# Optimization experiments

Hardware: AMD Instinct MI355X
Metric: run time of the kernel (lower is better)

The kernel has to match this reference:

```python
import jax, jax.numpy as jnp
import numpy as np

N_NODES = 100000
N_EDGES = 1600000
K = 3  # TAGConv default hops


def _make_lin(key, out_dim, in_dim):
    # K+1 bias-free linears (stacked) + one shared output bias, per PyG TAGConv
    kw, = jax.random.split(key, 1)
    scale = 1.0 / np.sqrt(in_dim)
    W = jax.random.uniform(kw, (K + 1, out_dim, in_dim), jnp.float32, -scale, scale)
    b = jnp.zeros((out_dim,), jnp.float32)
    return W, b


def setup_inputs() -> dict:
    key = jax.random.key(0)
    ks = jax.random.split(key, 6)
    x = jax.random.normal(ks[0], (N_NODES, 128), jnp.float32)
    edge_index = jax.random.randint(ks[1], (2, N_EDGES), 0, N_NODES, jnp.int64)
    W1, b1 = _make_lin(ks[2], 128, 128)
    W2, b2 = _make_lin(ks[3], 64, 128)
    W3, b3 = _make_lin(ks[4], 16, 64)
    return {"x": x, "edge_index": edge_index, "W1": W1, "b1": b1,
            "W2": W2, "b2": b2, "W3": W3, "b3": b3}


def _tagconv(x, row, col, norm, W, b, n):
    # out = sum_k lin_k(A_norm^k x) + b ; message x_j*norm gathered at col
    out = jnp.einsum('nd,od->no', x, W[0])
    h = x
    for k in range(1, W.shape[0]):
        h = jax.ops.segment_sum(norm[:, None] * h[row], col, num_segments=n)
        out = out + jnp.einsum('nd,od->no', h, W[k])
    return out + b


def _dropout(x, key, p=0.5):
    keep = jax.random.bernoulli(key, 1.0 - p, x.shape)
    return jnp.where(keep, x / (1.0 - p), 0.0)


def reference(x, edge_index, W1, b1, W2, b2, W3, b3):
    n = x.shape[0]
    row, col = edge_index[0], edge_index[1]
    # gcn_norm without self-loops (TAGConv default)
    deg = jax.ops.segment_sum(jnp.ones(row.shape[0], x.dtype), col, num_segments=n)
    dis = jnp.where(deg > 0, 1.0 / jnp.sqrt(jnp.where(deg > 0, deg, 1.0)), 0.0)
    norm = dis[row] * dis[col]

    dk1, dk2 = jax.random.split(jax.random.key(42))
    h = _tagconv(x, row, col, norm, W1, b1, n)
    h = _dropout(h, dk1)
    h = _tagconv(h, row, col, norm, W2, b2, n)
    h = jax.nn.elu(h)
    h = _dropout(h, dk2)
    h = _tagconv(h, row, col, norm, W3, b3, n)
    return h
```

## Files before the change

### kernel.cpp

```cpp
#include <hip/hip_runtime.h>
#include <stdint.h>
#include <math.h>

#define N_NODES 100000
#define N_EDGES 1600000

typedef __bf16 bf16_t;
typedef __attribute__((ext_vector_type(4))) __bf16 bf16x4;
typedef __attribute__((ext_vector_type(8))) __bf16 bf16x8;
typedef __attribute__((ext_vector_type(4))) float f32x4;

__device__ __forceinline__ f32x4 mfma16(bf16x8 a, bf16x8 b, f32x4 c) {
  return __builtin_amdgcn_mfma_f32_16x16x32_bf16(a, b, c, 0, 0, 0);
}

__device__ __host__ __forceinline__ uint32_t rotl32(uint32_t v, int d) {
  return (v << d) | (v >> (32 - d));
}

__device__ __host__ __forceinline__ void threefry2x32(uint32_t k0, uint32_t k1,
                                                      uint32_t x0, uint32_t x1,
                                                      uint32_t& o0, uint32_t& o1) {
  uint32_t ks0 = k0, ks1 = k1, ks2 = k0 ^ k1 ^ 0x1BD11BDAu;
  x0 += ks0; x1 += ks1;
#define TF_R(r) { x0 += x1; x1 = rotl32(x1, r); x1 ^= x0; }
  TF_R(13) TF_R(15) TF_R(26) TF_R(6)
  x0 += ks1; x1 += ks2 + 1u;
  TF_R(17) TF_R(29) TF_R(16) TF_R(24)
  x0 += ks2; x1 += ks0 + 2u;
  TF_R(13) TF_R(15) TF_R(26) TF_R(6)
  x0 += ks0; x1 += ks1 + 3u;
  TF_R(17) TF_R(29) TF_R(16) TF_R(24)
  x0 += ks1; x1 += ks2 + 4u;
  TF_R(13) TF_R(15) TF_R(26) TF_R(6)
  x0 += ks2; x1 += ks0 + 5u;
#undef TF_R
  o0 = x0; o1 = x1;
}

__device__ __forceinline__ float drop_scale(uint32_t idx, uint32_t k0, uint32_t k1) {
  uint32_t o0, o1;
  threefry2x32(k0, k1, 0u, idx, o0, o1);
  uint32_t bits = o0 ^ o1;
  float u = __uint_as_float((bits >> 9) | 0x3f800000u) - 1.0f;
  return (u < 0.5f) ? 2.0f : 0.0f;
}

__global__ __launch_bounds__(256) void detect_kernel(const int* __restrict__ ei,
                                                     int* __restrict__ found_nonzero) {
  int idx = blockIdx.x * 256 + threadIdx.x;
  size_t j = (size_t)idx * 781;
  if (ei[2 * j + 1] != 0) atomicOr(found_nonzero, 1);
}

__device__ __forceinline__ int edge_row(const int* ei, bool i32, int e) {
  return i32 ? ei[e] : ei[2 * (size_t)e];
}
__device__ __forceinline__ int edge_col(const int* ei, bool i32, int e) {
  return i32 ? ei[N_EDGES + e] : ei[2 * ((size_t)N_EDGES + (size_t)e)];
}

__global__ __launch_bounds__(256) void deg_kernel(const int* __restrict__ ei,
                                                  const int* __restrict__ flag,
                                                  int* __restrict__ deg) {
  int e = blockIdx.x * 256 + threadIdx.x;
  if (e < N_EDGES) {
    bool i32 = *flag != 0;
    atomicAdd(&deg[edge_col(ei, i32, e)], 1);
  }
}

__global__ __launch_bounds__(256) void dis_kernel(const int* __restrict__ deg,
                                                  float* __restrict__ dis) {
  int n = blockIdx.x * 256 + threadIdx.x;
  if (n < N_NODES) {
    int d = deg[n];
    dis[n] = (d > 0) ? (1.0f / sqrtf((float)d)) : 0.0f;
  }
}

#define SCAN_NB 391
__global__ __launch_bounds__(256) void bsum_kernel(const int* __restrict__ deg,
                                                   int* __restrict__ bsum) {
  __shared__ int sh[256];
  int i = blockIdx.x * 256 + threadIdx.x;
  sh[threadIdx.x] = (i < N_NODES) ? deg[i] : 0;
  __syncthreads();
  for (int ofs = 128; ofs > 0; ofs >>= 1) {
    if (threadIdx.x < ofs) sh[threadIdx.x] += sh[threadIdx.x + ofs];
    __syncthreads();
  }
  if (threadIdx.x == 0) bsum[blockIdx.x] = sh[0];
}

__global__ __launch_bounds__(512) void bscan_kernel(const int* __restrict__ bsum,
                                                    int* __restrict__ boffs) {
  __shared__ int sh[512];
  int t = threadIdx.x;
  int v = (t < SCAN_NB) ? bsum[t] : 0;
  sh[t] = v;
  __syncthreads();
  for (int ofs = 1; ofs < 512; ofs <<= 1) {
    int u = (t >= ofs) ? sh[t - ofs] : 0;
    __syncthreads();
    sh[t] += u;
    __syncthreads();
  }
  if (t < SCAN_NB) boffs[t] = sh[t] - v;
  if (t == 0) boffs[SCAN_NB] = sh[SCAN_NB - 1];
}

__global__ __launch_bounds__(256) void rptr_kernel(const int* __restrict__ deg,
                                                   const int* __restrict__ boffs,
                                                   int* __restrict__ rptr) {
  __shared__ int sh[256];
  int i = blockIdx.x * 256 + threadIdx.x;
  int v = (i < N_NODES) ? deg[i] : 0;
  sh[threadIdx.x] = v;
  __syncthreads();
  for (int ofs = 1; ofs < 256; ofs <<= 1) {
    int u = (threadIdx.x >= ofs) ? sh[threadIdx.x - ofs] : 0;
    __syncthreads();
    sh[threadIdx.x] += u;
    __syncthreads();
  }
  if (i <= N_NODES) rptr[i] = boffs[blockIdx.x] + sh[threadIdx.x] - v;
}

#define NFILL 512
#define MB1 1563
#define RANGE_N 12500

__device__ void fill_range(int b, int tid, const int* __restrict__ ei,
                           const int* __restrict__ flag,
                           const float* __restrict__ dis,
                           const int* __restrict__ rptr,
                           int* cursor, int2* __restrict__ erec) {
  int g = b & 7;
  int gb = b >> 3;
  int lo = g * RANGE_N, hi = lo + RANGE_N;
  bool i32 = *flag != 0;
  for (int e = gb * 256 + tid; e < N_EDGES; e += 64 * 256) {
    int c = edge_col(ei, i32, e);
    if (c < lo || c >= hi) continue;
    int r = edge_row(ei, i32, e);
    int p = atomicAdd(&cursor[c], 1);
    erec[rptr[c] + p] = make_int2(r, __float_as_int(dis[r] * dis[c]));
  }
}

__global__ __launch_bounds__(256) void fused1_kernel(
    const int* __restrict__ ei, const int* __restrict__ flag,
    const float* __restrict__ dis, const int* __restrict__ rptr,
    int* cursor, int2* __restrict__ erec,
    const float* __restrict__ x, const float* __restrict__ W1f,
    const float* __restrict__ b1,
    float* __restrict__ y0, bf16_t* __restrict__ y1,
    bf16_t* __restrict__ y2, bf16_t* __restrict__ y3,
    const float* __restrict__ W2, const float* __restrict__ W3,
    bf16_t* __restrict__ Wb2, bf16_t* __restrict__ Wb3) {
  constexpr int DIN = 128, LDK = DIN + 8, KI = DIN / 32, NCH = 8;
  __shared__ bf16_t sm[2][64 * LDK];
  const int tid = threadIdx.x;
  int b = blockIdx.x;

  if (b < NFILL) {
    fill_range(b, tid, ei, flag, dis, rptr, cursor, erec);
    return;
  }
  b -= NFILL;
  if (b >= MB1) {
    for (int i = tid; i < 32768; i += 256) Wb2[i] = (bf16_t)W2[i];
    for (int i = tid; i < 4096; i += 256) Wb3[i] = (bf16_t)W3[i];
    return;
  }

  const int m0 = b * 64;
  union U4 { bf16_t b[4]; uint2 u; };
  union U8 { bf16_t b[8]; uint4 u; };
  {
    constexpr int NL = 64 * DIN / 4 / 256;
#pragma unroll
    for (int it = 0; it < NL; ++it) {
      int idx = tid + it * 256;
      int r = idx / (DIN / 4), cc = (idx % (DIN / 4)) * 4;
      int gm = m0 + r;
      float4 v = (gm < N_NODES) ? ((const float4*)x)[((size_t)gm * DIN + cc) >> 2]
                                : make_float4(0.f, 0.f, 0.f, 0.f);
      U4 hi, lo;
      hi.b[0] = (bf16_t)v.x; lo.b[0] = (bf16_t)(v.x - (float)hi.b[0]);
      hi.b[1] = (bf16_t)v.y; lo.b[1] = (bf16_t)(v.y - (float)hi.b[1]);
      hi.b[2] = (bf16_t)v.z; lo.b[2] = (bf16_t)(v.z - (float)hi.b[2]);
      hi.b[3] = (bf16_t)v.w; lo.b[3] = (bf16_t)(v.w - (float)hi.b[3]);
      *(uint2*)&sm[0][r * LDK + cc] = hi.u;
      *(uint2*)&sm[1][r * LDK + cc] = lo.u;
    }
  }
  __syncthreads();

  const int w = tid >> 6, lane = tid & 63;
  const int wm = w & 1, wn = w >> 1;
  const int quad = lane >> 4, lr = lane & 15;

  bf16x8 aH[2][KI], aL[2][KI];
#pragma unroll
  for (int mt = 0; mt < 2; ++mt)
#pragma unroll
    for (int ki = 0; ki < KI; ++ki) {
      int rowa = wm * 32 + mt * 16 + lr;
      int koff = ki * 32 + quad * 8;
      aH[mt][ki] = *(const bf16x8*)&sm[0][rowa * LDK + koff];
      aL[mt][ki] = *(const bf16x8*)&sm[1][rowa * LDK + koff];
    }
  __syncthreads();

  constexpr int NLB = 64 * DIN / 8 / 256;
  auto loadW = [&](int gr, int cc) -> uint4 {
    const float4* p = (const float4*)&W1f[(size_t)gr * DIN + cc];
    float4 a = p[0], bq = p[1];
    U8 t;
    t.b[0] = (bf16_t)a.x;  t.b[1] = (bf16_t)a.y;
    t.b[2] = (bf16_t)a.z;  t.b[3] = (bf16_t)a.w;
    t.b[4] = (bf16_t)bq.x; t.b[5] = (bf16_t)bq.y;
    t.b[6] = (bf16_t)bq.z; t.b[7] = (bf16_t)bq.w;
    return t.u;
  };
  uint4 wreg[NLB];
#pragma unroll
  for (int it = 0; it < NLB; ++it) {
    int idx = tid + it * 256;
    int r = idx / (DIN / 8), cc = (idx % (DIN / 8)) * 8;
    wreg[it] = loadW(r, cc);
    *(uint4*)&sm[0][r * LDK + cc] = wreg[it];
  }
  __syncthreads();

  for (int nc = 0; nc < NCH; ++nc) {
    int p = nc & 1;
    if (nc + 1 < NCH) {
#pragma unroll
      for (int it = 0; it < NLB; ++it) {
        int idx = tid + it * 256;
        int r = idx / (DIN / 8), cc = (idx % (DIN / 8)) * 8;
        wreg[it] = loadW((nc + 1) * 64 + r, cc);
      }
    }

    f32x4 acc[2][2] = {};
#pragma unroll
    for (int ki = 0; ki < KI; ++ki) {
      int koff = ki * 32 + quad * 8;
      bf16x8 bfr[2];
#pragma unroll
      for (int nt = 0; nt < 2; ++nt)
        bfr[nt] = *(const bf16x8*)&sm[p][(wn * 32 + nt * 16 + lr) * LDK + koff];
#pragma unroll
      for (int mt = 0; mt < 2; ++mt)
#pragma unroll
        for (int nt = 0; nt < 2; ++nt) {
          acc[mt][nt] = mfma16(bfr[nt], aH[mt][ki], acc[mt][nt]);
          acc[mt][nt] = mfma16(bfr[nt], aL[mt][ki], acc[mt][nt]);
        }
    }

    if (nc + 1 < NCH) {
#pragma unroll
      for (int it = 0; it < NLB; ++it) {
        int idx = tid + it * 256;
        int r = idx / (DIN / 8), cc = (idx % (DIN / 8)) * 8;
        *(uint4*)&sm[p ^ 1][r * LDK + cc] = wreg[it];
      }
    }
    __syncthreads();

    const int n0 = nc * 64;
#pragma unroll
    for (int mt = 0; mt < 2; ++mt) {
      int m = m0 + wm * 32 + mt * 16 + lr;
      if (m >= N_NODES) continue;
#pragma unroll
      for (int nt = 0; nt < 2; ++nt) {
        int nb = n0 + wn * 32 + nt * 16 + quad * 4;
        int k = nb >> 7;
        int o = nb & 127;
        size_t oi = (size_t)m * 128 + o;
        if (k == 0) {
          float4 bv = *(const float4*)&b1[o];
          *(float4*)&y0[oi] = make_float4(acc[mt][nt][0] + bv.x,
                                          acc[mt][nt][1] + bv.y,
                                          acc[mt][nt][2] + bv.z,
                                          acc[mt][nt][3] + bv.w);
        } else {
          bf16_t* yk = (k == 1) ? y1 : (k == 2) ? y2 : y3;
          bf16x4 bb;
          bb.x = (bf16_t)acc[mt][nt][0];
          bb.y = (bf16_t)acc[mt][nt][1];
          bb.z = (bf16_t)acc[mt][nt][2];
          bb.w = (bf16_t)acc[mt][nt][3];
          *(bf16x4*)(yk + oi) = bb;
        }
      }
    }
  }
}

template <int DIN, int LOG_DOUT, int NCH, bool YB>
__global__ __launch_bounds__(256) void matmul_mfma_kernel(
    const void* __restrict__ hA, const void* __restrict__ hAlo,
    const bf16_t* __restrict__ Wb, const float* __restrict__ bias,
    float* __restrict__ y0, void* __restrict__ y1,
    void* __restrict__ y2, void* __restrict__ y3) {
  constexpr int LDK = DIN + 8;
  constexpr int DOUT = 1 << LOG_DOUT;
  constexpr int KI = DIN / 32;
  __shared__ bf16_t sm[2][64 * LDK];
  const int m0 = blockIdx.x * 64;
  const int tid = threadIdx.x;

  {
    constexpr int NL = 64 * DIN / 8 / 256;
#pragma unroll
    for (int it = 0; it < NL; ++it) {
      int idx = tid + it * 256;
      int r = idx / (DIN / 8), cc = (idx % (DIN / 8)) * 8;
      int gm = m0 + r;
      uint4 vh = make_uint4(0, 0, 0, 0), vl = make_uint4(0, 0, 0, 0);
      if (gm < N_NODES) {
        vh = ((const uint4*)hA)[((size_t)gm * DIN + cc) >> 3];
        vl = ((const uint4*)hAlo)[((size_t)gm * DIN + cc) >> 3];
      }
      *(uint4*)&sm[0][r * LDK + cc] = vh;
      *(uint4*)&sm[1][r * LDK + cc] = vl;
    }
  }
  __syncthreads();

  const int w = tid >> 6, lane = tid & 63;
  const int wm = w & 1, wn = w >> 1;
  const int quad = lane >> 4, lr = lane & 15;

  bf16x8 aH[2][KI], aL[2][KI];
#pragma unroll
  for (int mt = 0; mt < 2; ++mt)
#pragma unroll
    for (int ki = 0; ki < KI; ++ki) {
      int rowa = wm * 32 + mt * 16 + lr;
      int koff = ki * 32 + quad * 8;
      aH[mt][ki] = *(const bf16x8*)&sm[0][rowa * LDK + koff];
      aL[mt][ki] = *(const bf16x8*)&sm[1][rowa * LDK + koff];
    }
  __syncthreads();

  constexpr int NLB = 64 * DIN / 8 / 256;
  uint4 wreg[NLB];
#pragma unroll
  for (int it = 0; it < NLB; ++it) {
    int idx = tid + it * 256;
    int r = idx / (DIN / 8), cc = (idx % (DIN / 8)) * 8;
    wreg[it] = ((const uint4*)Wb)[(((size_t)r) * DIN + cc) >> 3];
    *(uint4*)&sm[0][r * LDK + cc] = wreg[it];
  }
  __syncthreads();

  for (int nc = 0; nc < NCH; ++nc) {
    int p = nc & 1;
    if (nc + 1 < NCH) {
#pragma unroll
      for (int it = 0; it < NLB; ++it) {
        int idx = tid + it * 256;
        int r = idx / (DIN / 8), cc = (idx % (DIN / 8)) * 8;
        wreg[it] = ((const uint4*)Wb)[(((size_t)((nc + 1) * 64 + r)) * DIN + cc) >> 3];
      }
    }

    f32x4 acc[2][2] = {};
#pragma unroll
    for (int ki = 0; ki < KI; ++ki) {
      int koff = ki * 32 + quad * 8;
      bf16x8 bfr[2];
#pragma unroll
      for (int nt = 0; nt < 2; ++nt)
        bfr[nt] = *(const bf16x8*)&sm[p][(wn * 32 + nt * 16 + lr) * LDK + koff];
#pragma unroll
      for (int mt = 0; mt < 2; ++mt)
#pragma unroll
        for (int nt = 0; nt < 2; ++nt) {
          acc[mt][nt] = mfma16(bfr[nt], aH[mt][ki], acc[mt][nt]);
          acc[mt][nt] = mfma16(bfr[nt], aL[mt][ki], acc[mt][nt]);
        }
    }

    if (nc + 1 < NCH) {
#pragma unroll
      for (int it = 0; it < NLB; ++it) {
        int idx = tid + it * 256;
        int r = idx / (DIN / 8), cc = (idx % (DIN / 8)) * 8;
        *(uint4*)&sm[p ^ 1][r * LDK + cc] = wreg[it];
      }
    }
    __syncthreads();

    const int n0 = nc * 64;
#pragma unroll
    for (int mt = 0; mt < 2; ++mt) {
      int m = m0 + wm * 32 + mt * 16 + lr;
      if (m >= N_NODES) continue;
#pragma unroll
      for (int nt = 0; nt < 2; ++nt) {
        int nb = n0 + wn * 32 + nt * 16 + quad * 4;
        int k = nb >> LOG_DOUT;
        int o = nb & (DOUT - 1);
        size_t oi = (size_t)m * DOUT + o;
        if (k == 0) {
          float4 bv = *(const float4*)&bias[o];
          *(float4*)&y0[oi] = make_float4(acc[mt][nt][0] + bv.x,
                                          acc[mt][nt][1] + bv.y,
                                          acc[mt][nt][2] + bv.z,
                                          acc[mt][nt][3] + bv.w);
        } else {
          void* yk = (k == 1) ? y1 : (k == 2) ? y2 : y3;
          if (YB) {
            bf16x4 bb;
            bb.x = (bf16_t)acc[mt][nt][0];
            bb.y = (bf16_t)acc[mt][nt][1];
            bb.z = (bf16_t)acc[mt][nt][2];
            bb.w = (bf16_t)acc[mt][nt][3];
            *(bf16x4*)((bf16_t*)yk + oi) = bb;
          } else {
            *(f32x4*)((float*)yk + oi) = acc[mt][nt];
          }
        }
      }
    }
  }
}

template <int D, int EPI, bool ZBF, bool ABF, int OMODE>
__global__ __launch_bounds__(256) void prop_kernel(
    const void* __restrict__ zv, const void* __restrict__ addv,
    void* __restrict__ outv, void* __restrict__ outv2,
    const int* __restrict__ rptr, const int2* __restrict__ erec,
    uint32_t k0, uint32_t k1) {
  constexpr int LPN = D / 4;
  constexpr int NPB = 256 / LPN;
  int lane = threadIdx.x % LPN;
  int nsub = threadIdx.x / LPN;
  int c = blockIdx.x * NPB + nsub;
  if (c >= N_NODES) return;
  int e0 = rptr[c], e1 = rptr[c + 1];
  float a0 = 0.f, a1 = 0.f, a2 = 0.f, a3 = 0.f;

  auto ld = [&](int r, float v[4]) {
    if (ZBF) {
      bf16x4 t = ((const bf16x4*)zv)[(size_t)r * LPN + lane];
      v[0] = (float)t.x; v[1] = (float)t.y; v[2] = (float)t.z; v[3] = (float)t.w;
    } else {
      float4 t = ((const float4*)zv)[(size_t)r * LPN + lane];
      v[0] = t.x; v[1] = t.y; v[2] = t.z; v[3] = t.w;
    }
  };

  int e = e0;
  for (; e + 3 < e1; e += 4) {
    int2 q[4];
    float v[4][4];
#pragma unroll
    for (int j = 0; j < 4; ++j) q[j] = erec[e + j];
#pragma unroll
    for (int j = 0; j < 4; ++j) ld(q[j].x, v[j]);
#pragma unroll
    for (int j = 0; j < 4; ++j) {
      float wv = __int_as_float(q[j].y);
      a0 = fmaf(wv, v[j][0], a0);
      a1 = fmaf(wv, v[j][1], a1);
      a2 = fmaf(wv, v[j][2], a2);
      a3 = fmaf(wv, v[j][3], a3);
    }
  }
  for (; e < e1; ++e) {
    int2 q = erec[e];
    float wv = __int_as_float(q.y);
    float v[4];
    ld(q.x, v);
    a0 = fmaf(wv, v[0], a0);
    a1 = fmaf(wv, v[1], a1);
    a2 = fmaf(wv, v[2], a2);
    a3 = fmaf(wv, v[3], a3);
  }

  size_t pidx = (size_t)c * LPN + lane;
  uint32_t fidx = (uint32_t)c * D + 4 * lane;
  float ax[4];
  if (ABF) {
    bf16x4 t = ((const bf16x4*)addv)[pidx];
    ax[0] = (float)t.x; ax[1] = (float)t.y; ax[2] = (float)t.z; ax[3] = (float)t.w;
  } else {
    float4 t = ((const float4*)addv)[pidx];
    ax[0] = t.x; ax[1] = t.y; ax[2] = t.z; ax[3] = t.w;
  }
  float o[4] = {a0 + ax[0], a1 + ax[1], a2 + ax[2], a3 + ax[3]};
  if (EPI == 1) {
#pragma unroll
    for (int j = 0; j < 4; ++j) o[j] *= drop_scale(fidx + j, k0, k1);
  }
  if (EPI == 2) {
#pragma unroll
    for (int j = 0; j < 4; ++j) {
      o[j] = (o[j] > 0.f) ? o[j] : expm1f(o[j]);
      o[j] *= drop_scale(fidx + j, k0, k1);
    }
  }
  if (OMODE == 0) {
    ((float4*)outv)[pidx] = make_float4(o[0], o[1], o[2], o[3]);
  } else if (OMODE == 1) {
    bf16x4 bv;
    bv.x = (bf16_t)o[0]; bv.y = (bf16_t)o[1];
    bv.z = (bf16_t)o[2]; bv.w = (bf16_t)o[3];
    ((bf16x4*)outv)[pidx] = bv;
  } else {
    bf16x4 hv, lv;
    hv.x = (bf16_t)o[0]; hv.y = (bf16_t)o[1];
    hv.z = (bf16_t)o[2]; hv.w = (bf16_t)o[3];
    lv.x = (bf16_t)(o[0] - (float)hv.x);
    lv.y = (bf16_t)(o[1] - (float)hv.y);
    lv.z = (bf16_t)(o[2] - (float)hv.z);
    lv.w = (bf16_t)(o[3] - (float)hv.w);
    ((bf16x4*)outv)[pidx] = hv;
    ((bf16x4*)outv2)[pidx] = lv;
  }
}

extern "C" void kernel_launch(void* const* d_in, const int* in_sizes, int n_in,
                              void* d_out, int out_size, void* d_ws, size_t ws_size,
                              hipStream_t stream) {
  const float* x  = (const float*)d_in[0];
  const int*   ei = (const int*)d_in[1];
  const float* W1 = (const float*)d_in[2];
  const float* b1 = (const float*)d_in[3];
  const float* W2 = (const float*)d_in[4];
  const float* b2 = (const float*)d_in[5];
  const float* W3 = (const float*)d_in[6];
  const float* b3 = (const float*)d_in[7];
  float* out = (float*)d_out;

  char* ws = (char*)d_ws;
  size_t off = 0;
  auto alloc = [&](size_t bytes) -> char* {
    char* p = ws + off;
    off += (bytes + 255) & ~(size_t)255;
    return p;
  };
  int*   flag   = (int*)alloc(256);
  int*   deg    = (int*)alloc((size_t)N_NODES * 4);
  int*   cursor = (int*)alloc((size_t)N_NODES * 4);
  float* dis    = (float*)alloc((size_t)N_NODES * 4);
  int*   rptr   = (int*)alloc((size_t)(N_NODES + 1) * 4);
  int*   bsum   = (int*)alloc((size_t)(SCAN_NB + 1) * 4);
  int*   boffs  = (int*)alloc((size_t)(SCAN_NB + 1) * 4);
  int2*  erec   = (int2*)alloc((size_t)N_EDGES * 8);
  bf16_t* Wb2  = (bf16_t*)alloc(32768 * 2);
  bf16_t* Wb3  = (bf16_t*)alloc(4096 * 2);
  float*  R0  = (float*)alloc((size_t)N_NODES * 128 * 4);
  float*  R2  = (float*)alloc((size_t)N_NODES * 16 * 4);
  bf16_t* Zb0 = (bf16_t*)alloc((size_t)N_NODES * 128 * 2);
  bf16_t* Zb1 = (bf16_t*)alloc((size_t)N_NODES * 128 * 2);
  bf16_t* Bb1 = (bf16_t*)alloc((size_t)N_NODES * 128 * 2);
  bf16_t* Bb2 = (bf16_t*)alloc((size_t)N_NODES * 128 * 2);

  hipMemsetAsync(flag, 0, 256, stream);
  hipMemsetAsync(deg, 0, (size_t)N_NODES * 4, stream);
  hipMemsetAsync(cursor, 0, (size_t)N_NODES * 4, stream);

  detect_kernel<<<8, 256, 0, stream>>>(ei, flag);
  deg_kernel<<<(N_EDGES + 255) / 256, 256, 0, stream>>>(ei, flag, deg);
  dis_kernel<<<(N_NODES + 255) / 256, 256, 0, stream>>>(deg, dis);
  bsum_kernel<<<SCAN_NB, 256, 0, stream>>>(deg, bsum);
  bscan_kernel<<<1, 512, 0, stream>>>(bsum, boffs);
  rptr_kernel<<<SCAN_NB, 256, 0, stream>>>(deg, boffs, rptr);

  uint32_t d10, d11, d20, d21;
  threefry2x32(0u, 42u, 0u, 0u, d10, d11);
  threefry2x32(0u, 42u, 0u, 1u, d20, d21);

  const int MB = (N_NODES + 63) / 64;
  const int PB128 = (N_NODES + 7) / 8;
  const int PB64n = (N_NODES + 15) / 16;
  const int PB16n = (N_NODES + 63) / 64;

  fused1_kernel<<<NFILL + MB1 + 1, 256, 0, stream>>>(
      ei, flag, dis, rptr, cursor, erec,
      x, W1, b1, R0, Bb1, Bb2, Zb0, W2, W3, Wb2, Wb3);

  prop_kernel<128, 0, true, true, 1><<<PB128, 256, 0, stream>>>(
      Zb0, Bb2, Zb1, nullptr, rptr, erec, 0, 0);
  prop_kernel<128, 0, true, true, 1><<<PB128, 256, 0, stream>>>(
      Zb1, Bb1, Zb0, nullptr, rptr, erec, 0, 0);
  prop_kernel<128, 1, true, false, 2><<<PB128, 256, 0, stream>>>(
      Zb0, R0, Bb2, Bb1, rptr, erec, d10, d11);

  float*  R1f = R0;
  bf16_t* S0 = Zb0;
  bf16_t* S1 = Zb0 + (size_t)N_NODES * 64;
  bf16_t* S2 = Zb1;
  bf16_t* S3 = Zb1 + (size_t)N_NODES * 64;
  matmul_mfma_kernel<128, 6, 4, true><<<MB, 256, 0, stream>>>(
      Bb2, Bb1, Wb2, b2, R1f, S2, S3, S0);
  prop_kernel<64, 0, true, true, 1><<<PB64n, 256, 0, stream>>>(
      S0, S3, S1, nullptr, rptr, erec, 0, 0);
  prop_kernel<64, 0, true, true, 1><<<PB64n, 256, 0, stream>>>(
      S1, S2, S0, nullptr, rptr, erec, 0, 0);
  prop_kernel<64, 2, true, false, 2><<<PB64n, 256, 0, stream>>>(
      S0, R1f, S2, S3, rptr, erec, d20, d21);

  float*  z0f = R2;
  bf16_t* zb1 = Bb1;
  bf16_t* zb2 = Bb1 + (size_t)N_NODES * 16;
  bf16_t* zb3 = Bb1 + (size_t)N_NODES * 32;
  matmul_mfma_kernel<64, 4, 1, true><<<MB, 256, 0, stream>>>(
      S2, S3, Wb3, b3, z0f, zb1, zb2, zb3);
  prop_kernel<16, 0, true, true, 1><<<PB16n, 256, 0, stream>>>(
      zb3, zb2, zb2, nullptr, rptr, erec, 0, 0);
  prop_kernel<16, 0, true, true, 1><<<PB16n, 256, 0, stream>>>(
      zb2, zb1, zb1, nullptr, rptr, erec, 0, 0);
  prop_kernel<16, 0, true, false, 0><<<PB16n, 256, 0, stream>>>(
      zb1, z0f, out, nullptr, rptr, erec, 0, 0);

  (void)in_sizes; (void)n_in; (void)out_size; (void)ws_size;
}
```

Before: 797.4 us.

## Factor symmetric norm into per-node scaling and store row-only CSR edges

Splits the edge weight dis[r]*dis[c] into a pre-scale by dis on the source features and a post-scale by dis on the destination, so each CSR record holds only the source row index. This halves edge-record bandwidth in every propagation pass and removes the per-edge multiply, and the gather loop is unrolled to 8 edges. The range-partitioned fill that rescanned the edge list eight times becomes a single pass with one thread per edge. The scaled intermediates are rounded to bf16 after the extra dis factor, which slightly changes rounding behaviour, and the single-pass fill depends on the grid covering exactly N_EDGES edges.

```diff
diff --git a/kernel.cpp b/kernel.cpp
--- a/kernel.cpp
+++ b/kernel.cpp
@@ -127,32 +127,13 @@
   if (i <= N_NODES) rptr[i] = boffs[blockIdx.x] + sh[threadIdx.x] - v;
 }
 
-#define NFILL 512
 #define MB1 1563
-#define RANGE_N 12500
-
-__device__ void fill_range(int b, int tid, const int* __restrict__ ei,
-                           const int* __restrict__ flag,
-                           const float* __restrict__ dis,
-                           const int* __restrict__ rptr,
-                           int* cursor, int2* __restrict__ erec) {
-  int g = b & 7;
-  int gb = b >> 3;
-  int lo = g * RANGE_N, hi = lo + RANGE_N;
-  bool i32 = *flag != 0;
-  for (int e = gb * 256 + tid; e < N_EDGES; e += 64 * 256) {
-    int c = edge_col(ei, i32, e);
-    if (c < lo || c >= hi) continue;
-    int r = edge_row(ei, i32, e);
-    int p = atomicAdd(&cursor[c], 1);
-    erec[rptr[c] + p] = make_int2(r, __float_as_int(dis[r] * dis[c]));
-  }
-}
+#define FB  6250
 
 __global__ __launch_bounds__(256) void fused1_kernel(
     const int* __restrict__ ei, const int* __restrict__ flag,
     const float* __restrict__ dis, const int* __restrict__ rptr,
-    int* cursor, int2* __restrict__ erec,
+    int* cursor, int* __restrict__ erow,
     const float* __restrict__ x, const float* __restrict__ W1f,
     const float* __restrict__ b1,
     float* __restrict__ y0, bf16_t* __restrict__ y1,
@@ -164,14 +145,19 @@
   const int tid = threadIdx.x;
   int b = blockIdx.x;
 
-  if (b < NFILL) {
-    fill_range(b, tid, ei, flag, dis, rptr, cursor, erec);
-    return;
-  }
-  b -= NFILL;
   if (b >= MB1) {
-    for (int i = tid; i < 32768; i += 256) Wb2[i] = (bf16_t)W2[i];
-    for (int i = tid; i < 4096; i += 256) Wb3[i] = (bf16_t)W3[i];
+    int fb = b - MB1;
+    if (fb < FB) {
+      int e = fb * 256 + tid;
+      bool i32 = *flag != 0;
+      int c = edge_col(ei, i32, e);
+      int r = edge_row(ei, i32, e);
+      int p = atomicAdd(&cursor[c], 1);
+      erow[rptr[c] + p] = r;
+    } else {
+      for (int i = tid; i < 32768; i += 256) Wb2[i] = (bf16_t)W2[i];
+      for (int i = tid; i < 4096; i += 256) Wb3[i] = (bf16_t)W3[i];
+    }
     return;
   }
 
@@ -278,6 +264,7 @@
     for (int mt = 0; mt < 2; ++mt) {
       int m = m0 + wm * 32 + mt * 16 + lr;
       if (m >= N_NODES) continue;
+      float dm = dis[m];
 #pragma unroll
       for (int nt = 0; nt < 2; ++nt) {
         int nb = n0 + wn * 32 + nt * 16 + quad * 4;
@@ -292,11 +279,12 @@
                                           acc[mt][nt][3] + bv.w);
         } else {
           bf16_t* yk = (k == 1) ? y1 : (k == 2) ? y2 : y3;
+          float s = (k == 3) ? dm : 1.0f;
           bf16x4 bb;
-          bb.x = (bf16_t)acc[mt][nt][0];
-          bb.y = (bf16_t)acc[mt][nt][1];
-          bb.z = (bf16_t)acc[mt][nt][2];
-          bb.w = (bf16_t)acc[mt][nt][3];
+          bb.x = (bf16_t)(s * acc[mt][nt][0]);
+          bb.y = (bf16_t)(s * acc[mt][nt][1]);
+          bb.z = (bf16_t)(s * acc[mt][nt][2]);
+          bb.w = (bf16_t)(s * acc[mt][nt][3]);
           *(bf16x4*)(yk + oi) = bb;
         }
       }
@@ -308,6 +296,7 @@
 __global__ __launch_bounds__(256) void matmul_mfma_kernel(
     const void* __restrict__ hA, const void* __restrict__ hAlo,
     const bf16_t* __restrict__ Wb, const float* __restrict__ bias,
+    const float* __restrict__ dis,
     float* __restrict__ y0, void* __restrict__ y1,
     void* __restrict__ y2, void* __restrict__ y3) {
   constexpr int LDK = DIN + 8;
@@ -405,6 +394,7 @@
     for (int mt = 0; mt < 2; ++mt) {
       int m = m0 + wm * 32 + mt * 16 + lr;
       if (m >= N_NODES) continue;
+      float dm = dis[m];
 #pragma unroll
       for (int nt = 0; nt < 2; ++nt) {
         int nb = n0 + wn * 32 + nt * 16 + quad * 4;
@@ -419,15 +409,18 @@
                                           acc[mt][nt][3] + bv.w);
         } else {
           void* yk = (k == 1) ? y1 : (k == 2) ? y2 : y3;
+          float s = (k == 3) ? dm : 1.0f;
           if (YB) {
             bf16x4 bb;
-            bb.x = (bf16_t)acc[mt][nt][0];
-            bb.y = (bf16_t)acc[mt][nt][1];
-            bb.z = (bf16_t)acc[mt][nt][2];
-            bb.w = (bf16_t)acc[mt][nt][3];
+            bb.x = (bf16_t)(s * acc[mt][nt][0]);
+            bb.y = (bf16_t)(s * acc[mt][nt][1]);
+            bb.z = (bf16_t)(s * acc[mt][nt][2]);
+            bb.w = (bf16_t)(s * acc[mt][nt][3]);
             *(bf16x4*)((bf16_t*)yk + oi) = bb;
           } else {
-            *(f32x4*)((float*)yk + oi) = acc[mt][nt];
+            f32x4 sv = acc[mt][nt];
+            sv[0] *= s; sv[1] *= s; sv[2] *= s; sv[3] *= s;
+            *(f32x4*)((float*)yk + oi) = sv;
           }
         }
       }
@@ -439,7 +432,8 @@
 __global__ __launch_bounds__(256) void prop_kernel(
     const void* __restrict__ zv, const void* __restrict__ addv,
     void* __restrict__ outv, void* __restrict__ outv2,
-    const int* __restrict__ rptr, const int2* __restrict__ erec,
+    const int* __restrict__ rptr, const int* __restrict__ erow,
+    const float* __restrict__ dis,
     uint32_t k0, uint32_t k1) {
   constexpr int LPN = D / 4;
   constexpr int NPB = 256 / LPN;
@@ -461,35 +455,27 @@
   };
 
   int e = e0;
-  for (; e + 3 < e1; e += 4) {
-    int2 q[4];
-    float v[4][4];
-#pragma unroll
-    for (int j = 0; j < 4; ++j) q[j] = erec[e + j];
-#pragma unroll
-    for (int j = 0; j < 4; ++j) ld(q[j].x, v[j]);
-#pragma unroll
-    for (int j = 0; j < 4; ++j) {
-      float wv = __int_as_float(q[j].y);
-      a0 = fmaf(wv, v[j][0], a0);
-      a1 = fmaf(wv, v[j][1], a1);
-      a2 = fmaf(wv, v[j][2], a2);
-      a3 = fmaf(wv, v[j][3], a3);
+  for (; e + 7 < e1; e += 8) {
+    int r[8];
+    float v[8][4];
+#pragma unroll
+    for (int j = 0; j < 8; ++j) r[j] = erow[e + j];
+#pragma unroll
+    for (int j = 0; j < 8; ++j) ld(r[j], v[j]);
+#pragma unroll
+    for (int j = 0; j < 8; ++j) {
+      a0 += v[j][0]; a1 += v[j][1]; a2 += v[j][2]; a3 += v[j][3];
     }
   }
   for (; e < e1; ++e) {
-    int2 q = erec[e];
-    float wv = __int_as_float(q.y);
     float v[4];
-    ld(q.x, v);
-    a0 = fmaf(wv, v[0], a0);
-    a1 = fmaf(wv, v[1], a1);
-    a2 = fmaf(wv, v[2], a2);
-    a3 = fmaf(wv, v[3], a3);
+    ld(erow[e], v);
+    a0 += v[0]; a1 += v[1]; a2 += v[2]; a3 += v[3];
   }
 
   size_t pidx = (size_t)c * LPN + lane;
   uint32_t fidx = (uint32_t)c * D + 4 * lane;
+  float dc = dis[c];
   float ax[4];
   if (ABF) {
     bf16x4 t = ((const bf16x4*)addv)[pidx];
@@ -498,7 +484,8 @@
     float4 t = ((const float4*)addv)[pidx];
     ax[0] = t.x; ax[1] = t.y; ax[2] = t.z; ax[3] = t.w;
   }
-  float o[4] = {a0 + ax[0], a1 + ax[1], a2 + ax[2], a3 + ax[3]};
+  float o[4] = {fmaf(dc, a0, ax[0]), fmaf(dc, a1, ax[1]),
+                fmaf(dc, a2, ax[2]), fmaf(dc, a3, ax[3])};
   if (EPI == 1) {
 #pragma unroll
     for (int j = 0; j < 4; ++j) o[j] *= drop_scale(fidx + j, k0, k1);
@@ -514,8 +501,8 @@
     ((float4*)outv)[pidx] = make_float4(o[0], o[1], o[2], o[3]);
   } else if (OMODE == 1) {
     bf16x4 bv;
-    bv.x = (bf16_t)o[0]; bv.y = (bf16_t)o[1];
-    bv.z = (bf16_t)o[2]; bv.w = (bf16_t)o[3];
+    bv.x = (bf16_t)(dc * o[0]); bv.y = (bf16_t)(dc * o[1]);
+    bv.z = (bf16_t)(dc * o[2]); bv.w = (bf16_t)(dc * o[3]);
     ((bf16x4*)outv)[pidx] = bv;
   } else {
     bf16x4 hv, lv;
@@ -557,7 +544,7 @@
   int*   rptr   = (int*)alloc((size_t)(N_NODES + 1) * 4);
   int*   bsum   = (int*)alloc((size_t)(SCAN_NB + 1) * 4);
   int*   boffs  = (int*)alloc((size_t)(SCAN_NB + 1) * 4);
-  int2*  erec   = (int2*)alloc((size_t)N_EDGES * 8);
+  int*   erow   = (int*)alloc((size_t)N_EDGES * 4);
   bf16_t* Wb2  = (bf16_t*)alloc(32768 * 2);
   bf16_t* Wb3  = (bf16_t*)alloc(4096 * 2);
   float*  R0  = (float*)alloc((size_t)N_NODES * 128 * 4);
@@ -587,16 +574,16 @@
   const int PB64n = (N_NODES + 15) / 16;
   const int PB16n = (N_NODES + 63) / 64;
 
-  fused1_kernel<<<NFILL + MB1 + 1, 256, 0, stream>>>(
-      ei, flag, dis, rptr, cursor, erec,
+  fused1_kernel<<<MB1 + FB + 1, 256, 0, stream>>>(
+      ei, flag, dis, rptr, cursor, erow,
       x, W1, b1, R0, Bb1, Bb2, Zb0, W2, W3, Wb2, Wb3);
 
   prop_kernel<128, 0, true, true, 1><<<PB128, 256, 0, stream>>>(
-      Zb0, Bb2, Zb1, nullptr, rptr, erec, 0, 0);
+      Zb0, Bb2, Zb1, nullptr, rptr, erow, dis, 0, 0);
   prop_kernel<128, 0, true, true, 1><<<PB128, 256, 0, stream>>>(
-      Zb1, Bb1, Zb0, nullptr, rptr, erec, 0, 0);
+      Zb1, Bb1, Zb0, nullptr, rptr, erow, dis, 0, 0);
   prop_kernel<128, 1, true, false, 2><<<PB128, 256, 0, stream>>>(
-      Zb0, R0, Bb2, Bb1, rptr, erec, d10, d11);
+      Zb0, R0, Bb2, Bb1, rptr, erow, dis, d10, d11);
 
   float*  R1f = R0;
   bf16_t* S0 = Zb0;
@@ -604,26 +591,26 @@
   bf16_t* S2 = Zb1;
   bf16_t* S3 = Zb1 + (size_t)N_NODES * 64;
   matmul_mfma_kernel<128, 6, 4, true><<<MB, 256, 0, stream>>>(
-      Bb2, Bb1, Wb2, b2, R1f, S2, S3, S0);
+      Bb2, Bb1, Wb2, b2, dis, R1f, S2, S3, S0);
   prop_kernel<64, 0, true, true, 1><<<PB64n, 256, 0, stream>>>(
-      S0, S3, S1, nullptr, rptr, erec, 0, 0);
+      S0, S3, S1, nullptr, rptr, erow, dis, 0, 0);
   prop_kernel<64, 0, true, true, 1><<<PB64n, 256, 0, stream>>>(
-      S1, S2, S0, nullptr, rptr, erec, 0, 0);
+      S1, S2, S0, nullptr, rptr, erow, dis, 0, 0);
   prop_kernel<64, 2, true, false, 2><<<PB64n, 256, 0, stream>>>(
-      S0, R1f, S2, S3, rptr, erec, d20, d21);
+      S0, R1f, S2, S3, rptr, erow, dis, d20, d21);
 
   float*  z0f = R2;
   bf16_t* zb1 = Bb1;
   bf16_t* zb2 = Bb1 + (size_t)N_NODES * 16;
   bf16_t* zb3 = Bb1 + (size_t)N_NODES * 32;
   matmul_mfma_kernel<64, 4, 1, true><<<MB, 256, 0, stream>>>(
-      S2, S3, Wb3, b3, z0f, zb1, zb2, zb3);
+      S2, S3, Wb3, b3, dis, z0f, zb1, zb2, zb3);
   prop_kernel<16, 0, true, true, 1><<<PB16n, 256, 0, stream>>>(
-      zb3, zb2, zb2, nullptr, rptr, erec, 0, 0);
+      zb3, zb2, zb2, nullptr, rptr, erow, dis, 0, 0);
   prop_kernel<16, 0, true, true, 1><<<PB16n, 256, 0, stream>>>(
-      zb2, zb1, zb1, nullptr, rptr, erec, 0, 0);
+      zb2, zb1, zb1, nullptr, rptr, erow, dis, 0, 0);
   prop_kernel<16, 0, true, false, 0><<<PB16n, 256, 0, stream>>>(
-      zb1, z0f, out, nullptr, rptr, erec, 0, 0);
+      zb1, z0f, out, nullptr, rptr, erow, dis, 0, 0);
 
   (void)in_sizes; (void)n_in; (void)out_size; (void)ws_size;
 }
```

After: 765.9 us. 3.9% less time.
